# Kernel tuning notes

Measured on AMD Instinct MI355X. Metric: run time of the kernel, lower is better.

The kernel has to match this reference:

```python
import jax, jax.numpy as jnp
import numpy as np

NUM_GRAPHS = 1024


def setup_inputs() -> dict:
    key = jax.random.key(0)
    k1, k2, k3, k4 = jax.random.split(key, 4)
    N, D, H = 500000, 256, 128
    x = jax.random.normal(k1, (N, D), dtype=jnp.float32)
    # attention MLP params (Linear(D,H) -> ReLU -> Linear(H,1))
    W1 = jax.random.normal(k2, (D, H), dtype=jnp.float32) * (1.0 / np.sqrt(D))
    b1 = jnp.zeros((H,), dtype=jnp.float32)
    W2 = jax.random.normal(k3, (H, 1), dtype=jnp.float32) * (1.0 / np.sqrt(H))
    b2 = jnp.zeros((1,), dtype=jnp.float32)
    batch = jnp.sort(jax.random.randint(k4, (N,), 0, NUM_GRAPHS)).astype(jnp.int64)
    return {"x": x, "W1": W1, "b1": b1, "W2": W2, "b2": b2, "batch": batch}


def reference(x, W1, b1, W2, b2, batch):
    # attention MLP -> scalar score per node, softmax over ALL nodes (global, as in source)
    h = jax.nn.relu(x @ W1 + b1)            # [N, H]
    scores = h @ W2 + b2                    # [N, 1]
    attn = jax.nn.softmax(scores.ravel())[:, None]  # [N, 1], global softmax

    # attention-weighted sum per graph
    attn_pooled = jax.ops.segment_sum(x * attn, batch, num_segments=NUM_GRAPHS,
                                      indices_are_sorted=True)  # [G, D]
    # max pool per graph (all segments occupied given N >> G)
    max_pooled = jax.ops.segment_max(x, batch, num_segments=NUM_GRAPHS,
                                     indices_are_sorted=True)   # [G, D]
    # mean pool per graph: scatter-add + clamped counts
    sum_pooled = jax.ops.segment_sum(x, batch, num_segments=NUM_GRAPHS,
                                     indices_are_sorted=True)   # [G, D]
    counts = jnp.bincount(batch, length=NUM_GRAPHS).astype(x.dtype)
    counts = jnp.clip(counts, 1.0, None)[:, None]                # [G, 1]
    mean_pooled = sum_pooled / counts

    return jnp.concatenate([attn_pooled, max_pooled, mean_pooled], axis=-1)  # [G, 3D]
```

## Files before the change

kernel.cpp:

```cpp
#include <hip/hip_runtime.h>
#include <cmath>

#define D_IN 256
#define H_DIM 128
#define NUM_GRAPHS 1024
#define CHUNK 32
#define MAXSEG 2
#define REC_F 768

typedef __attribute__((ext_vector_type(8))) __bf16 bf16x8;
typedef __attribute__((ext_vector_type(4))) float f32x4;

__device__ inline void load_lds_16(const void* g, void* l) {
    __builtin_amdgcn_global_load_lds(
        (const __attribute__((address_space(1))) void*)g,
        (__attribute__((address_space(3))) void*)l, 16, 0, 0);
}

__device__ inline int lower_bound_i(const int* __restrict__ arr, int n, int val) {
    int lo = 0, hi = n;
    while (lo < hi) {
        int mid = (lo + hi) >> 1;
        if (arr[mid] < val) lo = mid + 1; else hi = mid;
    }
    return lo;
}

__global__ __launch_bounds__(256) void prep_kernel(
    const float* __restrict__ W1, const int* __restrict__ batch, int N, int NB,
    ushort* __restrict__ packed, int* __restrict__ bounds,
    int* __restrict__ cmeta) {
    int b = blockIdx.x;
    if (b < 16) {
        int tid = b * 256 + threadIdx.x;
        int nt = tid >> 9;
        int ks = (tid >> 6) & 7;
        int l = tid & 63;
        int col = nt * 16 + (l & 15);
        int kbase = ks * 32 + ((l >> 4) & 3) * 8;
#pragma unroll
        for (int i = 0; i < 8; ++i) {
            float v = W1[(size_t)(kbase + i) * H_DIM + col];
            __bf16 h = (__bf16)v;
            packed[(size_t)tid * 8 + i] = __builtin_bit_cast(unsigned short, h);
        }
    } else if (b < 21) {
        int i = (b - 16) * 256 + threadIdx.x;
        if (i <= NUM_GRAPHS) bounds[i] = lower_bound_i(batch, N, i);
    } else {
        int c = (b - 21) * 256 + threadIdx.x;
        if (c < NB) {
            long long base = (long long)c * CHUNK;
            long long last = base + CHUNK - 1;
            if (last >= N) last = N - 1;
            int g0 = batch[base];
            int gend = batch[last];
            int p = 0;
            if (g0 != gend) {
                int lo = 1, hi = (int)(last - base);
                while (lo < hi) {
                    int mid = (lo + hi) >> 1;
                    if (batch[base + mid] != g0) hi = mid; else lo = mid + 1;
                }
                p = lo;
            }
            cmeta[c] = p;
        }
    }
}

__global__ __launch_bounds__(256, 4) void fused_kernel(
    const float* __restrict__ x, const ushort* __restrict__ w1p,
    const float* __restrict__ b1, const float* __restrict__ W2,
    const float* __restrict__ b2, const int* __restrict__ cmeta,
    float* __restrict__ recs, float* __restrict__ zpart, int N) {
    int tid = threadIdx.x;
    int l = tid & 63;
    int w = tid >> 6;
    int r16 = l & 15;
    int kg = l >> 4;
    int blk = blockIdx.x;
    long long base = (long long)blk * CHUNK;
    int chunkN = (int)min((long long)CHUNK, (long long)N - base);

    __shared__ float sxf[CHUNK * D_IN];
    __shared__ float pscore[4][CHUNK];

    int meta = cmeta[blk];

#pragma unroll
    for (int k = 0; k < 8; ++k) {
        int row = k * 4 + w;
        long long grow = base + row;
        if (grow >= N) grow = N - 1;
        unsigned srcb = ((unsigned)(l * 16)) ^ ((unsigned)(row & 7) << 4);
        const float* src = x + grow * D_IN + (srcb >> 2);
        char* dst = (char*)sxf + (unsigned)(row * 1024 + l * 16);
        load_lds_16(src, dst);
    }

    bf16x8 breg0[8], breg1[8];
#pragma unroll
    for (int ks = 0; ks < 8; ++ks) {
        breg0[ks] = *(const bf16x8*)(w1p + ((size_t)((w * 2) * 8 + ks) * 64 + l) * 8);
        breg1[ks] = *(const bf16x8*)(w1p + ((size_t)((w * 2 + 1) * 8 + ks) * 64 + l) * 8);
    }

    float w2v[2], b1v[2];
#pragma unroll
    for (int q = 0; q < 2; ++q) {
        int c = (w * 2 + q) * 16 + r16;
        w2v[q] = W2[c];
        b1v[q] = b1[c];
    }
    float bb = b2[0];

    __syncthreads();

    f32x4 acc[2][2] = {};
#pragma unroll
    for (int ks = 0; ks < 8; ++ks) {
#pragma unroll
        for (int mt = 0; mt < 2; ++mt) {
            int row = mt * 16 + r16;
            unsigned swz = (unsigned)(row & 7) << 4;
            unsigned cb = (unsigned)(ks * 128 + kg * 32);
            f32x4 u0 = *(const f32x4*)((const char*)sxf + row * 1024 + (cb ^ swz));
            f32x4 u1 = *(const f32x4*)((const char*)sxf + row * 1024 + ((cb + 16) ^ swz));
            bf16x8 af;
#pragma unroll
            for (int i = 0; i < 4; ++i) {
                af[i] = (__bf16)u0[i];
                af[i + 4] = (__bf16)u1[i];
            }
            acc[mt][0] = __builtin_amdgcn_mfma_f32_16x16x32_bf16(af, breg0[ks], acc[mt][0], 0, 0, 0);
            acc[mt][1] = __builtin_amdgcn_mfma_f32_16x16x32_bf16(af, breg1[ks], acc[mt][1], 0, 0, 0);
        }
    }
#pragma unroll
    for (int mt = 0; mt < 2; ++mt) {
#pragma unroll
        for (int reg = 0; reg < 4; ++reg) {
            float p = fmaxf(acc[mt][0][reg] + b1v[0], 0.f) * w2v[0] +
                      fmaxf(acc[mt][1][reg] + b1v[1], 0.f) * w2v[1];
            p += __shfl_xor(p, 1, 64);
            p += __shfl_xor(p, 2, 64);
            p += __shfl_xor(p, 4, 64);
            p += __shfl_xor(p, 8, 64);
            if (r16 == 0) pscore[w][mt * 16 + kg * 4 + reg] = p;
        }
    }
    __syncthreads();

    float e_l = 0.f;
    if (l < CHUNK) {
        float s = pscore[0][l] + pscore[1][l] + pscore[2][l] + pscore[3][l] + bb;
        e_l = (l < chunkN) ? __expf(s) : 0.f;
    }
    if (w == 0) {
        float z = e_l;
        z += __shfl_xor(z, 1, 64);
        z += __shfl_xor(z, 2, 64);
        z += __shfl_xor(z, 4, 64);
        z += __shfl_xor(z, 8, 64);
        z += __shfl_xor(z, 16, 64);
        z += __shfl_xor(z, 32, 64);
        if (l == 0) zpart[blk] = z;
    }

    int cg = l & 15;
    int rg = l >> 4;
    unsigned cbyte = (unsigned)(w * 256 + cg * 16);

    if (meta == 0 && chunkN == CHUNK) {
        f32x4 asum = {0.f, 0.f, 0.f, 0.f};
        f32x4 ssum = {0.f, 0.f, 0.f, 0.f};
        f32x4 mx = {-INFINITY, -INFINITY, -INFINITY, -INFINITY};
#pragma unroll
        for (int j = 0; j < 8; ++j) {
            int row = rg + 4 * j;
            float wj = __shfl(e_l, row, 64);
            unsigned addr = (unsigned)(row * 1024) +
                            (cbyte ^ ((unsigned)(row & 7) << 4));
            f32x4 v = *(const f32x4*)((const char*)sxf + addr);
#pragma unroll
            for (int c = 0; c < 4; ++c) {
                asum[c] += v[c] * wj;
                ssum[c] += v[c];
                mx[c] = fmaxf(mx[c], v[c]);
            }
        }
#pragma unroll
        for (int c = 0; c < 4; ++c) {
            asum[c] += __shfl_xor(asum[c], 16, 64);
            asum[c] += __shfl_xor(asum[c], 32, 64);
            ssum[c] += __shfl_xor(ssum[c], 16, 64);
            ssum[c] += __shfl_xor(ssum[c], 32, 64);
            mx[c] = fmaxf(mx[c], __shfl_xor(mx[c], 16, 64));
            mx[c] = fmaxf(mx[c], __shfl_xor(mx[c], 32, 64));
        }
        if (rg == 0) {
            float* rb = recs + (size_t)(blk * MAXSEG) * REC_F;
            int co = w * 64 + cg * 4;
            *(f32x4*)(rb + co) = asum;
            *(f32x4*)(rb + 256 + co) = ssum;
            *(f32x4*)(rb + 512 + co) = mx;
        }
    } else {
        int nseg = meta ? 2 : 1;
        for (int sg = 0; sg < nseg; ++sg) {
            int sStart = (sg == 0) ? 0 : meta;
            int sEnd = (sg == nseg - 1) ? chunkN : meta;
            f32x4 asum = {0.f, 0.f, 0.f, 0.f};
            f32x4 ssum = {0.f, 0.f, 0.f, 0.f};
            f32x4 mx = {-INFINITY, -INFINITY, -INFINITY, -INFINITY};
#pragma unroll
            for (int j = 0; j < 8; ++j) {
                int row = rg + 4 * j;
                float wj = __shfl(e_l, row, 64);
                bool in = (row >= sStart) && (row < sEnd);
                unsigned addr = (unsigned)(row * 1024) +
                                (cbyte ^ ((unsigned)(row & 7) << 4));
                f32x4 v = *(const f32x4*)((const char*)sxf + addr);
                float wje = in ? wj : 0.f;
#pragma unroll
                for (int c = 0; c < 4; ++c) {
                    asum[c] += v[c] * wje;
                    ssum[c] += in ? v[c] : 0.f;
                    mx[c] = fmaxf(mx[c], in ? v[c] : -INFINITY);
                }
            }
#pragma unroll
            for (int c = 0; c < 4; ++c) {
                asum[c] += __shfl_xor(asum[c], 16, 64);
                asum[c] += __shfl_xor(asum[c], 32, 64);
                ssum[c] += __shfl_xor(ssum[c], 16, 64);
                ssum[c] += __shfl_xor(ssum[c], 32, 64);
                mx[c] = fmaxf(mx[c], __shfl_xor(mx[c], 16, 64));
                mx[c] = fmaxf(mx[c], __shfl_xor(mx[c], 32, 64));
            }
            if (rg == 0) {
                float* rb = recs + (size_t)(blk * MAXSEG + sg) * REC_F;
                int co = w * 64 + cg * 4;
                *(f32x4*)(rb + co) = asum;
                *(f32x4*)(rb + 256 + co) = ssum;
                *(f32x4*)(rb + 512 + co) = mx;
            }
        }
    }
}

__global__ __launch_bounds__(256) void combine_kernel(
    const float* __restrict__ recs, const int* __restrict__ bounds,
    const float* __restrict__ zpart, int nzp, float* __restrict__ out) {
    int g = blockIdx.x;
    int tid = threadIdx.x;

    __shared__ float szr[256];
    float z = 0.f;
    for (int i = tid; i < nzp; i += 256) z += zpart[i];
    szr[tid] = z;
    __syncthreads();
    for (int off = 128; off > 0; off >>= 1) {
        if (tid < off) szr[tid] += szr[tid + off];
        __syncthreads();
    }
    float invZ = 1.f / szr[0];

    int start = bounds[g];
    int end = bounds[g + 1];
    int cnt = end - start;

    float ew = 0.f, ss = 0.f, mxv = -INFINITY;
    if (cnt > 0) {
        int b0 = start / CHUNK, b1 = (end - 1) / CHUNK;
        int sg0 = (start % CHUNK == 0) ? 0 : 1;
        for (int b = b0; b <= b1; ++b) {
            int sg = (b == b0) ? sg0 : 0;
            const float* rb = recs + (size_t)(b * MAXSEG + sg) * REC_F;
            ew += rb[tid];
            ss += rb[256 + tid];
            mxv = fmaxf(mxv, rb[512 + tid]);
        }
    }
    size_t ob = (size_t)g * (3 * D_IN);
    out[ob + tid] = ew * invZ;
    out[ob + D_IN + tid] = (cnt > 0) ? mxv : 0.f;
    out[ob + 2 * D_IN + tid] = ss / (float)max(cnt, 1);
}

extern "C" void kernel_launch(void* const* d_in, const int* in_sizes, int n_in,
                              void* d_out, int out_size, void* d_ws, size_t ws_size,
                              hipStream_t stream) {
    const float* x = (const float*)d_in[0];
    const float* W1 = (const float*)d_in[1];
    const float* b1 = (const float*)d_in[2];
    const float* W2 = (const float*)d_in[3];
    const float* b2 = (const float*)d_in[4];
    const int* batch = (const int*)d_in[5];
    int N = in_sizes[0] / D_IN;
    float* out = (float*)d_out;
    int NB = (N + CHUNK - 1) / CHUNK;

    char* ws = (char*)d_ws;
    size_t off = 0;
    ushort* w1p = (ushort*)(ws + off);
    off += 8 * 8 * 64 * 8 * sizeof(ushort);
    off = (off + 255) & ~(size_t)255;
    int* bounds = (int*)(ws + off);
    off += (NUM_GRAPHS + 1) * sizeof(int);
    off = (off + 255) & ~(size_t)255;
    int* cmeta = (int*)(ws + off);
    off += (size_t)NB * sizeof(int);
    off = (off + 255) & ~(size_t)255;
    float* recs = (float*)(ws + off);
    off += (size_t)NB * MAXSEG * REC_F * sizeof(float);
    off = (off + 255) & ~(size_t)255;
    float* zpart = (float*)(ws + off);
    off += (size_t)NB * sizeof(float);

    int prepBlocks = 21 + (NB + 255) / 256;
    prep_kernel<<<prepBlocks, 256, 0, stream>>>(W1, batch, N, NB, w1p, bounds, cmeta);
    fused_kernel<<<NB, 256, 0, stream>>>(x, w1p, b1, W2, b2, cmeta,
                                         recs, zpart, N);
    combine_kernel<<<NUM_GRAPHS, 256, 0, stream>>>(recs, bounds, zpart, NB, out);
}
```

Before: 163.6 us.

## Split x tile load to overlap second half with first MFMA pass; hoist Z reduction

The fused kernel now issues async LDS loads for only the first 16 rows before the barrier, then loads the remaining 16 rows while computing MFMA scores on the first half, with an extra barrier before the second half. Separately, the global softmax denominator reduction, which every one of the 1024 combine blocks redundantly recomputed over ~15.6k partials, moves into a single-block kernel whose reciprocal the combine blocks then read. The first change aims to hide load latency. The second removes redundant reads and reductions at the cost of one more kernel launch. The mid-compute barrier relies on the second batch of async loads completing before it, which is not obviously guaranteed by an explicit wait.

```diff
diff --git a/kernel.cpp b/kernel.cpp
--- a/kernel.cpp
+++ b/kernel.cpp
@@ -89,14 +89,13 @@
     int meta = cmeta[blk];
 
 #pragma unroll
-    for (int k = 0; k < 8; ++k) {
+    for (int k = 0; k < 4; ++k) {
         int row = k * 4 + w;
         long long grow = base + row;
         if (grow >= N) grow = N - 1;
         unsigned srcb = ((unsigned)(l * 16)) ^ ((unsigned)(row & 7) << 4);
-        const float* src = x + grow * D_IN + (srcb >> 2);
-        char* dst = (char*)sxf + (unsigned)(row * 1024 + l * 16);
-        load_lds_16(src, dst);
+        load_lds_16(x + grow * D_IN + (srcb >> 2),
+                    (char*)sxf + (unsigned)(row * 1024 + l * 16));
     }
 
     bf16x8 breg0[8], breg1[8];
@@ -105,7 +104,6 @@
         breg0[ks] = *(const bf16x8*)(w1p + ((size_t)((w * 2) * 8 + ks) * 64 + l) * 8);
         breg1[ks] = *(const bf16x8*)(w1p + ((size_t)((w * 2 + 1) * 8 + ks) * 64 + l) * 8);
     }
-
     float w2v[2], b1v[2];
 #pragma unroll
     for (int q = 0; q < 2; ++q) {
@@ -117,39 +115,73 @@
 
     __syncthreads();
 
+#pragma unroll
+    for (int k = 4; k < 8; ++k) {
+        int row = k * 4 + w;
+        long long grow = base + row;
+        if (grow >= N) grow = N - 1;
+        unsigned srcb = ((unsigned)(l * 16)) ^ ((unsigned)(row & 7) << 4);
+        load_lds_16(x + grow * D_IN + (srcb >> 2),
+                    (char*)sxf + (unsigned)(row * 1024 + l * 16));
+    }
+
     f32x4 acc[2][2] = {};
 #pragma unroll
     for (int ks = 0; ks < 8; ++ks) {
-#pragma unroll
-        for (int mt = 0; mt < 2; ++mt) {
-            int row = mt * 16 + r16;
-            unsigned swz = (unsigned)(row & 7) << 4;
-            unsigned cb = (unsigned)(ks * 128 + kg * 32);
-            f32x4 u0 = *(const f32x4*)((const char*)sxf + row * 1024 + (cb ^ swz));
-            f32x4 u1 = *(const f32x4*)((const char*)sxf + row * 1024 + ((cb + 16) ^ swz));
-            bf16x8 af;
-#pragma unroll
-            for (int i = 0; i < 4; ++i) {
-                af[i] = (__bf16)u0[i];
-                af[i + 4] = (__bf16)u1[i];
-            }
-            acc[mt][0] = __builtin_amdgcn_mfma_f32_16x16x32_bf16(af, breg0[ks], acc[mt][0], 0, 0, 0);
-            acc[mt][1] = __builtin_amdgcn_mfma_f32_16x16x32_bf16(af, breg1[ks], acc[mt][1], 0, 0, 0);
-        }
-    }
-#pragma unroll
-    for (int mt = 0; mt < 2; ++mt) {
-#pragma unroll
-        for (int reg = 0; reg < 4; ++reg) {
-            float p = fmaxf(acc[mt][0][reg] + b1v[0], 0.f) * w2v[0] +
-                      fmaxf(acc[mt][1][reg] + b1v[1], 0.f) * w2v[1];
-            p += __shfl_xor(p, 1, 64);
-            p += __shfl_xor(p, 2, 64);
-            p += __shfl_xor(p, 4, 64);
-            p += __shfl_xor(p, 8, 64);
-            if (r16 == 0) pscore[w][mt * 16 + kg * 4 + reg] = p;
-        }
-    }
+        int row = r16;
+        unsigned swz = (unsigned)(row & 7) << 4;
+        unsigned cb = (unsigned)(ks * 128 + kg * 32);
+        f32x4 u0 = *(const f32x4*)((const char*)sxf + row * 1024 + (cb ^ swz));
+        f32x4 u1 = *(const f32x4*)((const char*)sxf + row * 1024 + ((cb + 16) ^ swz));
+        bf16x8 af;
+#pragma unroll
+        for (int i = 0; i < 4; ++i) {
+            af[i] = (__bf16)u0[i];
+            af[i + 4] = (__bf16)u1[i];
+        }
+        acc[0][0] = __builtin_amdgcn_mfma_f32_16x16x32_bf16(af, breg0[ks], acc[0][0], 0, 0, 0);
+        acc[0][1] = __builtin_amdgcn_mfma_f32_16x16x32_bf16(af, breg1[ks], acc[0][1], 0, 0, 0);
+    }
+#pragma unroll
+    for (int reg = 0; reg < 4; ++reg) {
+        float p = fmaxf(acc[0][0][reg] + b1v[0], 0.f) * w2v[0] +
+                  fmaxf(acc[0][1][reg] + b1v[1], 0.f) * w2v[1];
+        p += __shfl_xor(p, 1, 64);
+        p += __shfl_xor(p, 2, 64);
+        p += __shfl_xor(p, 4, 64);
+        p += __shfl_xor(p, 8, 64);
+        if (r16 == 0) pscore[w][kg * 4 + reg] = p;
+    }
+
+    __syncthreads();
+
+#pragma unroll
+    for (int ks = 0; ks < 8; ++ks) {
+        int row = 16 + r16;
+        unsigned swz = (unsigned)(row & 7) << 4;
+        unsigned cb = (unsigned)(ks * 128 + kg * 32);
+        f32x4 u0 = *(const f32x4*)((const char*)sxf + row * 1024 + (cb ^ swz));
+        f32x4 u1 = *(const f32x4*)((const char*)sxf + row * 1024 + ((cb + 16) ^ swz));
+        bf16x8 af;
+#pragma unroll
+        for (int i = 0; i < 4; ++i) {
+            af[i] = (__bf16)u0[i];
+            af[i + 4] = (__bf16)u1[i];
+        }
+        acc[1][0] = __builtin_amdgcn_mfma_f32_16x16x32_bf16(af, breg0[ks], acc[1][0], 0, 0, 0);
+        acc[1][1] = __builtin_amdgcn_mfma_f32_16x16x32_bf16(af, breg1[ks], acc[1][1], 0, 0, 0);
+    }
+#pragma unroll
+    for (int reg = 0; reg < 4; ++reg) {
+        float p = fmaxf(acc[1][0][reg] + b1v[0], 0.f) * w2v[0] +
+                  fmaxf(acc[1][1][reg] + b1v[1], 0.f) * w2v[1];
+        p += __shfl_xor(p, 1, 64);
+        p += __shfl_xor(p, 2, 64);
+        p += __shfl_xor(p, 4, 64);
+        p += __shfl_xor(p, 8, 64);
+        if (r16 == 0) pscore[w][16 + kg * 4 + reg] = p;
+    }
+
     __syncthreads();
 
     float e_l = 0.f;
@@ -250,22 +282,27 @@
     }
 }
 
+__global__ __launch_bounds__(256) void zreduce_kernel(
+    const float* __restrict__ zpart, int n, float* __restrict__ MZ) {
+    int tid = threadIdx.x;
+    float z = 0.f;
+    for (int i = tid; i < n; i += 256) z += zpart[i];
+    __shared__ float sz[256];
+    sz[tid] = z;
+    __syncthreads();
+    for (int off = 128; off > 0; off >>= 1) {
+        if (tid < off) sz[tid] += sz[tid + off];
+        __syncthreads();
+    }
+    if (tid == 0) MZ[0] = 1.f / sz[0];
+}
+
 __global__ __launch_bounds__(256) void combine_kernel(
     const float* __restrict__ recs, const int* __restrict__ bounds,
-    const float* __restrict__ zpart, int nzp, float* __restrict__ out) {
+    const float* __restrict__ MZ, float* __restrict__ out) {
     int g = blockIdx.x;
     int tid = threadIdx.x;
-
-    __shared__ float szr[256];
-    float z = 0.f;
-    for (int i = tid; i < nzp; i += 256) z += zpart[i];
-    szr[tid] = z;
-    __syncthreads();
-    for (int off = 128; off > 0; off >>= 1) {
-        if (tid < off) szr[tid] += szr[tid + off];
-        __syncthreads();
-    }
-    float invZ = 1.f / szr[0];
+    float invZ = MZ[0];
 
     int start = bounds[g];
     int end = bounds[g + 1];
@@ -318,10 +355,14 @@
     off = (off + 255) & ~(size_t)255;
     float* zpart = (float*)(ws + off);
     off += (size_t)NB * sizeof(float);
+    off = (off + 255) & ~(size_t)255;
+    float* MZ = (float*)(ws + off);
+    off += 256;
 
     int prepBlocks = 21 + (NB + 255) / 256;
     prep_kernel<<<prepBlocks, 256, 0, stream>>>(W1, batch, N, NB, w1p, bounds, cmeta);
     fused_kernel<<<NB, 256, 0, stream>>>(x, w1p, b1, W2, b2, cmeta,
                                          recs, zpart, N);
-    combine_kernel<<<NUM_GRAPHS, 256, 0, stream>>>(recs, bounds, zpart, NB, out);
-}
+    zreduce_kernel<<<1, 256, 0, stream>>>(zpart, NB, MZ);
+    combine_kernel<<<NUM_GRAPHS, 256, 0, stream>>>(recs, bounds, MZ, out);
+}
```

New measurement: 187.1 us. 1.14x slower.
